# Optimization experiments

Hardware: AMD Instinct MI355X
Metric: run time of the kernel (lower is better)

Reference implementation:

```python
import jax, jax.numpy as jnp
import numpy as np

N_USERS = 100000
N_ITEMS = 50000
EMB_DIM = 64
N_LAYERS = 2
N_INTENTS = 128
N_EDGES = 4000000
N_NODES = N_USERS + N_ITEMS


def setup_inputs() -> dict:
    key = jax.random.key(0)
    k1, k2, k3, k4, k5 = jax.random.split(key, 5)
    return {
        "user_emb": 0.1 * jax.random.normal(k1, (N_USERS, EMB_DIM), dtype=jnp.float32),
        "item_emb": 0.1 * jax.random.normal(k2, (N_ITEMS, EMB_DIM), dtype=jnp.float32),
        "intents": jax.random.normal(k3, (EMB_DIM, N_INTENTS), dtype=jnp.float32) * (2.0 / (EMB_DIM + N_INTENTS)) ** 0.5,
        "h_idx": jax.random.randint(k4, (N_EDGES,), 0, N_NODES, dtype=jnp.int64)
        if jax.config.jax_enable_x64 else jax.random.randint(k4, (N_EDGES,), 0, N_NODES, dtype=jnp.int32),
        "t_idx": jax.random.randint(k5, (N_EDGES,), 0, N_NODES, dtype=jnp.int32),
    }


def _spmm(h_idx, t_idx, g_vals, x):
    # y[h] += g_vals * x[t]  (sparse matrix @ dense, COO form)
    gathered = x[t_idx] * g_vals[:, None]  # [E, D]
    return jax.ops.segment_sum(gathered, h_idx, num_segments=N_NODES)


def reference(user_emb, item_emb, intents, h_idx, t_idx):
    # --- _cal_sparse_adj: G = D^{-1/2} A D^{-1/2}, A values are ones ---
    deg = jax.ops.segment_sum(jnp.ones_like(h_idx, dtype=user_emb.dtype), h_idx,
                              num_segments=N_NODES)
    d_inv_sqrt = jnp.where(deg > 0, jax.lax.rsqrt(jnp.maximum(deg, 1e-12)), 0.0)
    g_vals = d_inv_sqrt[h_idx] * d_inv_sqrt[t_idx]  # [E]

    # --- multi-layer propagation with intent-aware embeddings ---
    embs = jnp.concatenate([user_emb, item_emb], axis=0)  # [N, D]
    all_embs = [embs]
    for _ in range(N_LAYERS):
        gnn_embs = _spmm(h_idx, t_idx, g_vals, embs)  # [N, D]
        # intent projection: softmax over intents, reconstruct in emb space
        u, it = embs[:N_USERS], embs[N_USERS:]
        u_int = jax.nn.softmax(u @ intents, axis=1) @ intents.T      # [n_users, D]
        i_int = jax.nn.softmax(it @ intents, axis=1) @ intents.T     # [n_items, D]
        int_embs = jnp.concatenate([u_int, i_int], axis=0)
        embs = gnn_embs + int_embs
        all_embs.append(embs)
    out = jnp.sum(jnp.stack(all_embs, axis=1), axis=1) / len(all_embs)  # mean over layers
    return out
```

## Files before the change

kernel.cpp:

```cpp
#include <hip/hip_runtime.h>
#include <math.h>

#define N_USERS 100000
#define N_ITEMS 50000
#define N_NODES 150000
#define EMB 64
#define NI 128
#define NUM_EDGES 4000000
#define NPAD 150016
#define NB 586
#define BSTRIDE 8192
#define ETILE 4096
#define EGRID ((NUM_EDGES + ETILE - 1) / ETILE)
#define NTILES (N_NODES / 16)
#define SBLK ((NTILES + 7) / 8)

typedef __attribute__((ext_vector_type(8))) short bf16x8;
typedef __attribute__((ext_vector_type(4))) float f32x4;

__device__ __forceinline__ unsigned short f2bf(float f) {
    unsigned int u = __float_as_uint(f);
    u += 0x7FFFu + ((u >> 16) & 1u);
    return (unsigned short)(u >> 16);
}
__device__ __forceinline__ float bflo(unsigned int u) { return __uint_as_float(u << 16); }
__device__ __forceinline__ float bfhi(unsigned int u) { return __uint_as_float(u & 0xFFFF0000u); }


__global__ __launch_bounds__(256) void bucket_scatter(const int* __restrict__ h,
                                                      const int* __restrict__ t,
                                                      int* __restrict__ gcur,
                                                      unsigned int* __restrict__ ebuf) {
    __shared__ int lc[NB];
    __shared__ int lbase[NB];
    __shared__ int lcur[NB];
    int tid = threadIdx.x;
    for (int i = tid; i < NB; i += 256) lc[i] = 0;
    __syncthreads();
    int base = blockIdx.x * ETILE;
#pragma unroll
    for (int k = 0; k < ETILE / 256; ++k) {
        int idx = base + k * 256 + tid;
        if (idx < NUM_EDGES) atomicAdd(&lc[h[idx] >> 8], 1);
    }
    __syncthreads();
    for (int i = tid; i < NB; i += 256) {
        int c = lc[i];
        lbase[i] = c ? (i * BSTRIDE + atomicAdd(&gcur[i], c)) : 0;
        lcur[i] = 0;
    }
    __syncthreads();
#pragma unroll
    for (int k = 0; k < ETILE / 256; ++k) {
        int idx = base + k * 256 + tid;
        if (idx < NUM_EDGES) {
            int hh = h[idx], tt = t[idx];
            int b = hh >> 8;
            int p = lbase[b] + atomicAdd(&lcur[b], 1);
            int lim = b * BSTRIDE + BSTRIDE - 1;
            p = (p <= lim) ? p : lim;
            ebuf[p] = ((unsigned int)(hh & 255) << 18) | (unsigned int)tt;
        }
    }
}


__global__ __launch_bounds__(256) void bucket_csr(const int* __restrict__ gcur,
                                                  unsigned int* __restrict__ ebuf,
                                                  int2* __restrict__ rmeta,
                                                  float* __restrict__ dinv) {
    __shared__ unsigned int in_s[BSTRIDE];
    __shared__ unsigned int out_s[BSTRIDE];
    __shared__ int cnt_s[256];
    __shared__ int base_s[256];
    __shared__ int sc[256];
    int b = blockIdx.x, tid = threadIdx.x;
    int s = b * BSTRIDE;
    int n = gcur[b];
    if (n > BSTRIDE) n = BSTRIDE;

    for (int i = tid; i < n; i += 256) in_s[i] = ebuf[s + i];
    cnt_s[tid] = 0;
    __syncthreads();
    for (int i = tid; i < n; i += 256) atomicAdd(&cnt_s[in_s[i] >> 18], 1);
    __syncthreads();

    int c = cnt_s[tid];
    sc[tid] = c;
    __syncthreads();
    for (int off = 1; off < 256; off <<= 1) {
        int tv = (tid >= off) ? sc[tid - off] : 0;
        __syncthreads();
        sc[tid] += tv;
        __syncthreads();
    }
    int excl = sc[tid] - c;
    base_s[tid] = excl;
    int node = (b << 8) + tid;
    rmeta[node] = make_int2(s + excl, c);
    dinv[node] = (c > 0) ? rsqrtf((float)c) : 0.0f;
    cnt_s[tid] = 0;
    __syncthreads();

    for (int i = tid; i < n; i += 256) {
        unsigned int q = in_s[i];
        int hl = (int)(q >> 18);
        int p = base_s[hl] + atomicAdd(&cnt_s[hl], 1);
        out_s[p] = q & 0x3FFFFu;
    }
    __syncthreads();
    for (int i = tid; i < n; i += 256) ebuf[s + i] = out_s[i];
}


__global__ void init_kernel(const float4* __restrict__ ue4, const float4* __restrict__ ie4,
                            uint2* __restrict__ ebf4, float4* __restrict__ out4) {
    int i = blockIdx.x * blockDim.x + threadIdx.x;
    const int uelems = N_USERS * EMB / 4;
    const int total  = N_NODES * EMB / 4;
    if (i < total) {
        float4 v = (i < uelems) ? ue4[i] : ie4[i - uelems];
        out4[i] = v;
        unsigned int p0 = ((unsigned int)f2bf(v.y) << 16) | f2bf(v.x);
        unsigned int p1 = ((unsigned int)f2bf(v.w) << 16) | f2bf(v.z);
        ebf4[i] = make_uint2(p0, p1);
    }
}


__global__ __launch_bounds__(512, 6) void spmm_intent(const int2* __restrict__ rmeta,
                                                      const unsigned int* __restrict__ col,
                                                      const float* __restrict__ dinv,
                                                      const unsigned short* __restrict__ ebf,
                                                      unsigned short* __restrict__ ebfout,
                                                      const float* __restrict__ W,
                                                      float* __restrict__ acc, float scale) {
    __shared__ __align__(16) unsigned short W1s[NI * 72];
    __shared__ __align__(16) unsigned short W2s[EMB * 136];
    __shared__ __align__(16) float UPool[8][520];

    int tid = threadIdx.x;

    const float4* W4 = (const float4*)W;
#pragma unroll
    for (int k = 0; k < 4; ++k) {
        int f = tid + k * 512;
        float4 v = W4[f];
        int d = f >> 5, c4 = (f & 31) << 2;
        unsigned short bx = f2bf(v.x), by = f2bf(v.y), bz = f2bf(v.z), bw = f2bf(v.w);
        *(unsigned int*)&W2s[d * 136 + c4]     = (unsigned int)bx | ((unsigned int)by << 16);
        *(unsigned int*)&W2s[d * 136 + c4 + 2] = (unsigned int)bz | ((unsigned int)bw << 16);
        W1s[(c4 + 0) * 72 + d] = bx;
        W1s[(c4 + 1) * 72 + d] = by;
        W1s[(c4 + 2) * 72 + d] = bz;
        W1s[(c4 + 3) * 72 + d] = bw;
    }
    __syncthreads();

    int wid = tid >> 6, lane = tid & 63;
    int q = lane >> 4, c = lane & 15;
    int qq = lane >> 3, cc = lane & 7;
    int tile = blockIdx.x * 8 + wid;
    if (tile >= NTILES) return;
    int rowbase = tile << 4;
    unsigned short* pw = (unsigned short*)&UPool[wid][0];
    float* fw = &UPool[wid][0];

    const unsigned short* erow = ebf + ((size_t)(rowbase + c) << 6);
    bf16x8 A0 = *(const bf16x8*)(erow + (q << 3));
    bf16x8 A1 = *(const bf16x8*)(erow + 32 + (q << 3));
    f32x4 S[8];
#pragma unroll
    for (int t = 0; t < 8; ++t) {
        bf16x8 B0 = *(const bf16x8*)&W1s[(16 * t + c) * 72 + (q << 3)];
        bf16x8 B1 = *(const bf16x8*)&W1s[(16 * t + c) * 72 + 32 + (q << 3)];
        f32x4 z = {0.f, 0.f, 0.f, 0.f};
        z = __builtin_amdgcn_mfma_f32_16x16x32_bf16(A0, B0, z, 0, 0, 0);
        S[t] = __builtin_amdgcn_mfma_f32_16x16x32_bf16(A1, B1, z, 0, 0, 0);
    }

#pragma unroll
    for (int r = 0; r < 4; ++r) {
        float m = S[0][r];
#pragma unroll
        for (int t = 1; t < 8; ++t) m = fmaxf(m, S[t][r]);
        m = fmaxf(m, __shfl_xor(m, 1)); m = fmaxf(m, __shfl_xor(m, 2));
        m = fmaxf(m, __shfl_xor(m, 4)); m = fmaxf(m, __shfl_xor(m, 8));
        float sum = 0.f;
#pragma unroll
        for (int t = 0; t < 8; ++t) { float ex = __expf(S[t][r] - m); S[t][r] = ex; sum += ex; }
        sum += __shfl_xor(sum, 1); sum += __shfl_xor(sum, 2);
        sum += __shfl_xor(sum, 4); sum += __shfl_xor(sum, 8);
        float inv = 1.0f / sum;
#pragma unroll
        for (int t = 0; t < 8; ++t) S[t][r] *= inv;
    }

    f32x4 O0 = {0.f, 0.f, 0.f, 0.f}, O1 = O0, O2 = O0, O3 = O0;
#pragma unroll
    for (int s2 = 0; s2 < 4; ++s2) {
#pragma unroll
        for (int h2 = 0; h2 < 2; ++h2) {
            int t = 2 * s2 + h2;
#pragma unroll
            for (int r = 0; r < 4; ++r) {
                float p = S[t][r];
                unsigned short b = f2bf(p);
                pw[(4 * q + r) * 40 + (h2 << 4) + c] = b;
                S[t][r] = p - bflo((unsigned int)b);
            }
        }
        bf16x8 Pf = *(const bf16x8*)&pw[c * 40 + (q << 3)];
        {
            bf16x8 Bf0 = *(const bf16x8*)&W2s[(c) * 136 + (s2 << 5) + (q << 3)];
            bf16x8 Bf1 = *(const bf16x8*)&W2s[(16 + c) * 136 + (s2 << 5) + (q << 3)];
            bf16x8 Bf2 = *(const bf16x8*)&W2s[(32 + c) * 136 + (s2 << 5) + (q << 3)];
            bf16x8 Bf3 = *(const bf16x8*)&W2s[(48 + c) * 136 + (s2 << 5) + (q << 3)];
            O0 = __builtin_amdgcn_mfma_f32_16x16x32_bf16(Pf, Bf0, O0, 0, 0, 0);
            O1 = __builtin_amdgcn_mfma_f32_16x16x32_bf16(Pf, Bf1, O1, 0, 0, 0);
            O2 = __builtin_amdgcn_mfma_f32_16x16x32_bf16(Pf, Bf2, O2, 0, 0, 0);
            O3 = __builtin_amdgcn_mfma_f32_16x16x32_bf16(Pf, Bf3, O3, 0, 0, 0);
        }
#pragma unroll
        for (int h2 = 0; h2 < 2; ++h2) {
            int t = 2 * s2 + h2;
#pragma unroll
            for (int r = 0; r < 4; ++r)
                pw[(4 * q + r) * 40 + (h2 << 4) + c] = f2bf(S[t][r]);
        }
        bf16x8 Pl = *(const bf16x8*)&pw[c * 40 + (q << 3)];
        {
            bf16x8 Bf0 = *(const bf16x8*)&W2s[(c) * 136 + (s2 << 5) + (q << 3)];
            bf16x8 Bf1 = *(const bf16x8*)&W2s[(16 + c) * 136 + (s2 << 5) + (q << 3)];
            bf16x8 Bf2 = *(const bf16x8*)&W2s[(32 + c) * 136 + (s2 << 5) + (q << 3)];
            bf16x8 Bf3 = *(const bf16x8*)&W2s[(48 + c) * 136 + (s2 << 5) + (q << 3)];
            O0 = __builtin_amdgcn_mfma_f32_16x16x32_bf16(Pl, Bf0, O0, 0, 0, 0);
            O1 = __builtin_amdgcn_mfma_f32_16x16x32_bf16(Pl, Bf1, O1, 0, 0, 0);
            O2 = __builtin_amdgcn_mfma_f32_16x16x32_bf16(Pl, Bf2, O2, 0, 0, 0);
            O3 = __builtin_amdgcn_mfma_f32_16x16x32_bf16(Pl, Bf3, O3, 0, 0, 0);
        }
    }

    asm volatile("" ::: "memory");

#pragma unroll 1
    for (int half = 0; half < 2; ++half) {
        int row = rowbase + half * 8 + qq;
        int2 rm = rmeta[row];
        int s = rm.x, deg = rm.y;
        float dr = dinv[row];
        int dm = deg;
        dm = max(dm, __shfl_xor(dm, 8));
        dm = max(dm, __shfl_xor(dm, 16));
        dm = max(dm, __shfl_xor(dm, 32));
        dm = __builtin_amdgcn_readfirstlane(dm);

        float a0 = 0.f, a1 = 0.f, a2 = 0.f, a3 = 0.f;
        float a4 = 0.f, a5 = 0.f, a6 = 0.f, a7 = 0.f;
        int last = s + ((deg > 0) ? (deg - 1) : 0);
        int i1 = s + 1; if (i1 > last) i1 = last;
        int ce0 = (int)col[s];
        int ce1 = (int)col[i1];
        float g0 = dinv[ce0], g1 = dinv[ce1];
        const unsigned short* eb = ebf + (cc << 3);
        for (int it = 0; it < dm; it += 2) {
            float gu0 = (it < deg) ? g0 : 0.f;
            float gu1 = (it + 1 < deg) ? g1 : 0.f;
            uint4 u0 = *(const uint4*)(eb + ((size_t)ce0 << 6));
            uint4 u1 = *(const uint4*)(eb + ((size_t)ce1 << 6));
            int p0 = s + it + 2; if (p0 > last) p0 = last;
            int p1 = s + it + 3; if (p1 > last) p1 = last;
            ce0 = (int)col[p0]; ce1 = (int)col[p1];
            g0 = dinv[ce0]; g1 = dinv[ce1];
            a0 = fmaf(gu0, bflo(u0.x), a0); a1 = fmaf(gu0, bfhi(u0.x), a1);
            a2 = fmaf(gu0, bflo(u0.y), a2); a3 = fmaf(gu0, bfhi(u0.y), a3);
            a4 = fmaf(gu0, bflo(u0.z), a4); a5 = fmaf(gu0, bfhi(u0.z), a5);
            a6 = fmaf(gu0, bflo(u0.w), a6); a7 = fmaf(gu0, bfhi(u0.w), a7);
            a0 = fmaf(gu1, bflo(u1.x), a0); a1 = fmaf(gu1, bfhi(u1.x), a1);
            a2 = fmaf(gu1, bflo(u1.y), a2); a3 = fmaf(gu1, bfhi(u1.y), a3);
            a4 = fmaf(gu1, bflo(u1.z), a4); a5 = fmaf(gu1, bfhi(u1.z), a5);
            a6 = fmaf(gu1, bflo(u1.w), a6); a7 = fmaf(gu1, bfhi(u1.w), a7);
        }
        int fb = qq * 65 + (cc << 3);
        fw[fb + 0] = a0 * dr; fw[fb + 1] = a1 * dr;
        fw[fb + 2] = a2 * dr; fw[fb + 3] = a3 * dr;
        fw[fb + 4] = a4 * dr; fw[fb + 5] = a5 * dr;
        fw[fb + 6] = a6 * dr; fw[fb + 7] = a7 * dr;

        if ((q >> 1) == half) {
            int qb = (q & 1) << 2;
#pragma unroll
            for (int r = 0; r < 4; ++r) {
                int rl = qb + r;
                const float* gr = &fw[rl * 65];
                size_t rbase = ((size_t)(rowbase + half * 8 + rl) << 6);
                float nv0 = gr[c]      + O0[r];
                float nv1 = gr[16 + c] + O1[r];
                float nv2 = gr[32 + c] + O2[r];
                float nv3 = gr[48 + c] + O3[r];
                ebfout[rbase + c]      = f2bf(nv0);
                ebfout[rbase + 16 + c] = f2bf(nv1);
                ebfout[rbase + 32 + c] = f2bf(nv2);
                ebfout[rbase + 48 + c] = f2bf(nv3);
                acc[rbase + c]      = (acc[rbase + c]      + nv0) * scale;
                acc[rbase + 16 + c] = (acc[rbase + 16 + c] + nv1) * scale;
                acc[rbase + 32 + c] = (acc[rbase + 32 + c] + nv2) * scale;
                acc[rbase + 48 + c] = (acc[rbase + 48 + c] + nv3) * scale;
            }
        }
    }
}


extern "C" void kernel_launch(void* const* d_in, const int* in_sizes, int n_in,
                              void* d_out, int out_size, void* d_ws, size_t ws_size,
                              hipStream_t stream) {
    const float* ue = (const float*)d_in[0];
    const float* ie = (const float*)d_in[1];
    const float* W  = (const float*)d_in[2];
    const int*   h  = (const int*)d_in[3];
    const int*   t  = (const int*)d_in[4];
    float* out = (float*)d_out;

    int*            gcur  = (int*)d_ws;
    int2*           rmeta = (int2*)(gcur + 1024);
    float*          dinv  = (float*)(rmeta + NPAD);
    unsigned int*   ebuf  = (unsigned int*)(dinv + NPAD);
    unsigned short* ebfA  = (unsigned short*)(ebuf + NB * BSTRIDE);
    unsigned short* ebfB  = ebfA + (size_t)NPAD * EMB;

    hipMemsetAsync(gcur, 0, NB * sizeof(int), stream);
    bucket_scatter<<<EGRID, 256, 0, stream>>>(h, t, gcur, ebuf);
    bucket_csr<<<NB, 256, 0, stream>>>(gcur, ebuf, rmeta, dinv);
    init_kernel<<<(N_NODES * EMB / 4 + 255) / 256, 256, 0, stream>>>(
        (const float4*)ue, (const float4*)ie, (uint2*)ebfA, (float4*)out);

    const unsigned int* col = ebuf;
    spmm_intent<<<SBLK, 512, 0, stream>>>(rmeta, col, dinv, ebfA, ebfB, W, out, 1.0f);
    spmm_intent<<<SBLK, 512, 0, stream>>>(rmeta, col, dinv, ebfB, ebfA, W, out, 1.0f / 3.0f);
}
```

Baseline: 435.9 us.

## Replace bucketed CSR build with atomic degree count and placement; move weights to global bf16

The two-pass bucketed CSR construction is replaced by a per-node degree-count kernel, a per-bucket scan kernel, and a direct atomic placement kernel. Intent weights are converted to bf16 once in a separate kernel and read from global memory instead of being staged into shared memory by every block. The spmm kernel now uses 256-thread blocks, unrolls the gather loop by four with clamped column indices, and runs the intent MFMA after the neighbour gather. Global atomics on per-node counters add contention and make edge order within a row nondeterministic. Dropping shared-memory weights cuts per-block setup but adds global/L2 traffic for weight fragments.

```diff
diff --git a/kernel.cpp b/kernel.cpp
--- a/kernel.cpp
+++ b/kernel.cpp
@@ -10,10 +10,9 @@
 #define NPAD 150016
 #define NB 586
 #define BSTRIDE 8192
-#define ETILE 4096
-#define EGRID ((NUM_EDGES + ETILE - 1) / ETILE)
 #define NTILES (N_NODES / 16)
-#define SBLK ((NTILES + 7) / 8)
+#define SBLK ((NTILES + 3) / 4)
+#define EDGE_BLOCKS ((NUM_EDGES + 255) / 256)
 
 typedef __attribute__((ext_vector_type(8))) short bf16x8;
 typedef __attribute__((ext_vector_type(4))) float f32x4;
@@ -27,65 +26,19 @@
 __device__ __forceinline__ float bfhi(unsigned int u) { return __uint_as_float(u & 0xFFFF0000u); }
 
 
-__global__ __launch_bounds__(256) void bucket_scatter(const int* __restrict__ h,
-                                                      const int* __restrict__ t,
-                                                      int* __restrict__ gcur,
-                                                      unsigned int* __restrict__ ebuf) {
-    __shared__ int lc[NB];
-    __shared__ int lbase[NB];
-    __shared__ int lcur[NB];
-    int tid = threadIdx.x;
-    for (int i = tid; i < NB; i += 256) lc[i] = 0;
-    __syncthreads();
-    int base = blockIdx.x * ETILE;
-#pragma unroll
-    for (int k = 0; k < ETILE / 256; ++k) {
-        int idx = base + k * 256 + tid;
-        if (idx < NUM_EDGES) atomicAdd(&lc[h[idx] >> 8], 1);
-    }
-    __syncthreads();
-    for (int i = tid; i < NB; i += 256) {
-        int c = lc[i];
-        lbase[i] = c ? (i * BSTRIDE + atomicAdd(&gcur[i], c)) : 0;
-        lcur[i] = 0;
-    }
-    __syncthreads();
-#pragma unroll
-    for (int k = 0; k < ETILE / 256; ++k) {
-        int idx = base + k * 256 + tid;
-        if (idx < NUM_EDGES) {
-            int hh = h[idx], tt = t[idx];
-            int b = hh >> 8;
-            int p = lbase[b] + atomicAdd(&lcur[b], 1);
-            int lim = b * BSTRIDE + BSTRIDE - 1;
-            p = (p <= lim) ? p : lim;
-            ebuf[p] = ((unsigned int)(hh & 255) << 18) | (unsigned int)tt;
-        }
-    }
-}
-
-
-__global__ __launch_bounds__(256) void bucket_csr(const int* __restrict__ gcur,
-                                                  unsigned int* __restrict__ ebuf,
-                                                  int2* __restrict__ rmeta,
-                                                  float* __restrict__ dinv) {
-    __shared__ unsigned int in_s[BSTRIDE];
-    __shared__ unsigned int out_s[BSTRIDE];
-    __shared__ int cnt_s[256];
-    __shared__ int base_s[256];
+__global__ __launch_bounds__(256) void deg_count(const int* __restrict__ h,
+                                                 int* __restrict__ deg) {
+    int i = blockIdx.x * 256 + threadIdx.x;
+    if (i < NUM_EDGES) atomicAdd(&deg[h[i]], 1);
+}
+
+__global__ __launch_bounds__(256) void node_meta(int* __restrict__ deg,
+                                                 int2* __restrict__ rmeta,
+                                                 float* __restrict__ dinv) {
     __shared__ int sc[256];
     int b = blockIdx.x, tid = threadIdx.x;
-    int s = b * BSTRIDE;
-    int n = gcur[b];
-    if (n > BSTRIDE) n = BSTRIDE;
-
-    for (int i = tid; i < n; i += 256) in_s[i] = ebuf[s + i];
-    cnt_s[tid] = 0;
-    __syncthreads();
-    for (int i = tid; i < n; i += 256) atomicAdd(&cnt_s[in_s[i] >> 18], 1);
-    __syncthreads();
-
-    int c = cnt_s[tid];
+    int node = (b << 8) + tid;
+    int c = (node < N_NODES) ? deg[node] : 0;
     sc[tid] = c;
     __syncthreads();
     for (int off = 1; off < 256; off <<= 1) {
@@ -94,22 +47,23 @@
         sc[tid] += tv;
         __syncthreads();
     }
-    int excl = sc[tid] - c;
-    base_s[tid] = excl;
-    int node = (b << 8) + tid;
-    rmeta[node] = make_int2(s + excl, c);
-    dinv[node] = (c > 0) ? rsqrtf((float)c) : 0.0f;
-    cnt_s[tid] = 0;
-    __syncthreads();
-
-    for (int i = tid; i < n; i += 256) {
-        unsigned int q = in_s[i];
-        int hl = (int)(q >> 18);
-        int p = base_s[hl] + atomicAdd(&cnt_s[hl], 1);
-        out_s[p] = q & 0x3FFFFu;
-    }
-    __syncthreads();
-    for (int i = tid; i < n; i += 256) ebuf[s + i] = out_s[i];
+    int start = b * BSTRIDE + (sc[tid] - c);
+    if (node < N_NODES) {
+        rmeta[node] = make_int2(start, c);
+        dinv[node] = (c > 0) ? rsqrtf((float)c) : 0.0f;
+        deg[node] = start;
+    }
+}
+
+__global__ __launch_bounds__(256) void place(const int* __restrict__ h,
+                                             const int* __restrict__ t,
+                                             int* __restrict__ cur,
+                                             unsigned int* __restrict__ ebuf) {
+    int i = blockIdx.x * 256 + threadIdx.x;
+    if (i < NUM_EDGES) {
+        int p = atomicAdd(&cur[h[i]], 1);
+        ebuf[p] = (unsigned int)t[i];
+    }
 }
 
 
@@ -128,120 +82,38 @@
 }
 
 
-__global__ __launch_bounds__(512, 6) void spmm_intent(const int2* __restrict__ rmeta,
+__global__ __launch_bounds__(256) void wconv(const float* __restrict__ W,
+                                             unsigned short* __restrict__ Wt,
+                                             unsigned short* __restrict__ W2b) {
+    int i = blockIdx.x * 256 + threadIdx.x;
+    if (i < EMB * NI) {
+        int d = i >> 7, c = i & 127;
+        unsigned short b = f2bf(W[i]);
+        W2b[i] = b;
+        Wt[c * EMB + d] = b;
+    }
+}
+
+
+__global__ __launch_bounds__(256, 7) void spmm_intent(const int2* __restrict__ rmeta,
                                                       const unsigned int* __restrict__ col,
                                                       const float* __restrict__ dinv,
                                                       const unsigned short* __restrict__ ebf,
                                                       unsigned short* __restrict__ ebfout,
-                                                      const float* __restrict__ W,
+                                                      const unsigned short* __restrict__ Wt,
+                                                      const unsigned short* __restrict__ W2b,
                                                       float* __restrict__ acc, float scale) {
-    __shared__ __align__(16) unsigned short W1s[NI * 72];
-    __shared__ __align__(16) unsigned short W2s[EMB * 136];
-    __shared__ __align__(16) float UPool[8][520];
+    __shared__ __align__(16) float UPool[4][1408];
 
     int tid = threadIdx.x;
-
-    const float4* W4 = (const float4*)W;
-#pragma unroll
-    for (int k = 0; k < 4; ++k) {
-        int f = tid + k * 512;
-        float4 v = W4[f];
-        int d = f >> 5, c4 = (f & 31) << 2;
-        unsigned short bx = f2bf(v.x), by = f2bf(v.y), bz = f2bf(v.z), bw = f2bf(v.w);
-        *(unsigned int*)&W2s[d * 136 + c4]     = (unsigned int)bx | ((unsigned int)by << 16);
-        *(unsigned int*)&W2s[d * 136 + c4 + 2] = (unsigned int)bz | ((unsigned int)bw << 16);
-        W1s[(c4 + 0) * 72 + d] = bx;
-        W1s[(c4 + 1) * 72 + d] = by;
-        W1s[(c4 + 2) * 72 + d] = bz;
-        W1s[(c4 + 3) * 72 + d] = bw;
-    }
-    __syncthreads();
-
     int wid = tid >> 6, lane = tid & 63;
     int q = lane >> 4, c = lane & 15;
     int qq = lane >> 3, cc = lane & 7;
-    int tile = blockIdx.x * 8 + wid;
+    int tile = blockIdx.x * 4 + wid;
     if (tile >= NTILES) return;
     int rowbase = tile << 4;
-    unsigned short* pw = (unsigned short*)&UPool[wid][0];
     float* fw = &UPool[wid][0];
-
-    const unsigned short* erow = ebf + ((size_t)(rowbase + c) << 6);
-    bf16x8 A0 = *(const bf16x8*)(erow + (q << 3));
-    bf16x8 A1 = *(const bf16x8*)(erow + 32 + (q << 3));
-    f32x4 S[8];
-#pragma unroll
-    for (int t = 0; t < 8; ++t) {
-        bf16x8 B0 = *(const bf16x8*)&W1s[(16 * t + c) * 72 + (q << 3)];
-        bf16x8 B1 = *(const bf16x8*)&W1s[(16 * t + c) * 72 + 32 + (q << 3)];
-        f32x4 z = {0.f, 0.f, 0.f, 0.f};
-        z = __builtin_amdgcn_mfma_f32_16x16x32_bf16(A0, B0, z, 0, 0, 0);
-        S[t] = __builtin_amdgcn_mfma_f32_16x16x32_bf16(A1, B1, z, 0, 0, 0);
-    }
-
-#pragma unroll
-    for (int r = 0; r < 4; ++r) {
-        float m = S[0][r];
-#pragma unroll
-        for (int t = 1; t < 8; ++t) m = fmaxf(m, S[t][r]);
-        m = fmaxf(m, __shfl_xor(m, 1)); m = fmaxf(m, __shfl_xor(m, 2));
-        m = fmaxf(m, __shfl_xor(m, 4)); m = fmaxf(m, __shfl_xor(m, 8));
-        float sum = 0.f;
-#pragma unroll
-        for (int t = 0; t < 8; ++t) { float ex = __expf(S[t][r] - m); S[t][r] = ex; sum += ex; }
-        sum += __shfl_xor(sum, 1); sum += __shfl_xor(sum, 2);
-        sum += __shfl_xor(sum, 4); sum += __shfl_xor(sum, 8);
-        float inv = 1.0f / sum;
-#pragma unroll
-        for (int t = 0; t < 8; ++t) S[t][r] *= inv;
-    }
-
-    f32x4 O0 = {0.f, 0.f, 0.f, 0.f}, O1 = O0, O2 = O0, O3 = O0;
-#pragma unroll
-    for (int s2 = 0; s2 < 4; ++s2) {
-#pragma unroll
-        for (int h2 = 0; h2 < 2; ++h2) {
-            int t = 2 * s2 + h2;
-#pragma unroll
-            for (int r = 0; r < 4; ++r) {
-                float p = S[t][r];
-                unsigned short b = f2bf(p);
-                pw[(4 * q + r) * 40 + (h2 << 4) + c] = b;
-                S[t][r] = p - bflo((unsigned int)b);
-            }
-        }
-        bf16x8 Pf = *(const bf16x8*)&pw[c * 40 + (q << 3)];
-        {
-            bf16x8 Bf0 = *(const bf16x8*)&W2s[(c) * 136 + (s2 << 5) + (q << 3)];
-            bf16x8 Bf1 = *(const bf16x8*)&W2s[(16 + c) * 136 + (s2 << 5) + (q << 3)];
-            bf16x8 Bf2 = *(const bf16x8*)&W2s[(32 + c) * 136 + (s2 << 5) + (q << 3)];
-            bf16x8 Bf3 = *(const bf16x8*)&W2s[(48 + c) * 136 + (s2 << 5) + (q << 3)];
-            O0 = __builtin_amdgcn_mfma_f32_16x16x32_bf16(Pf, Bf0, O0, 0, 0, 0);
-            O1 = __builtin_amdgcn_mfma_f32_16x16x32_bf16(Pf, Bf1, O1, 0, 0, 0);
-            O2 = __builtin_amdgcn_mfma_f32_16x16x32_bf16(Pf, Bf2, O2, 0, 0, 0);
-            O3 = __builtin_amdgcn_mfma_f32_16x16x32_bf16(Pf, Bf3, O3, 0, 0, 0);
-        }
-#pragma unroll
-        for (int h2 = 0; h2 < 2; ++h2) {
-            int t = 2 * s2 + h2;
-#pragma unroll
-            for (int r = 0; r < 4; ++r)
-                pw[(4 * q + r) * 40 + (h2 << 4) + c] = f2bf(S[t][r]);
-        }
-        bf16x8 Pl = *(const bf16x8*)&pw[c * 40 + (q << 3)];
-        {
-            bf16x8 Bf0 = *(const bf16x8*)&W2s[(c) * 136 + (s2 << 5) + (q << 3)];
-            bf16x8 Bf1 = *(const bf16x8*)&W2s[(16 + c) * 136 + (s2 << 5) + (q << 3)];
-            bf16x8 Bf2 = *(const bf16x8*)&W2s[(32 + c) * 136 + (s2 << 5) + (q << 3)];
-            bf16x8 Bf3 = *(const bf16x8*)&W2s[(48 + c) * 136 + (s2 << 5) + (q << 3)];
-            O0 = __builtin_amdgcn_mfma_f32_16x16x32_bf16(Pl, Bf0, O0, 0, 0, 0);
-            O1 = __builtin_amdgcn_mfma_f32_16x16x32_bf16(Pl, Bf1, O1, 0, 0, 0);
-            O2 = __builtin_amdgcn_mfma_f32_16x16x32_bf16(Pl, Bf2, O2, 0, 0, 0);
-            O3 = __builtin_amdgcn_mfma_f32_16x16x32_bf16(Pl, Bf3, O3, 0, 0, 0);
-        }
-    }
-
-    asm volatile("" ::: "memory");
+    unsigned short* pw = (unsigned short*)&UPool[wid][1088];
 
 #pragma unroll 1
     for (int half = 0; half < 2; ++half) {
@@ -258,20 +130,28 @@
         float a0 = 0.f, a1 = 0.f, a2 = 0.f, a3 = 0.f;
         float a4 = 0.f, a5 = 0.f, a6 = 0.f, a7 = 0.f;
         int last = s + ((deg > 0) ? (deg - 1) : 0);
-        int i1 = s + 1; if (i1 > last) i1 = last;
-        int ce0 = (int)col[s];
-        int ce1 = (int)col[i1];
-        float g0 = dinv[ce0], g1 = dinv[ce1];
+        int ce0 = min((int)col[s], N_NODES - 1);
+        int ce1 = min((int)col[min(s + 1, last)], N_NODES - 1);
+        int ce2 = min((int)col[min(s + 2, last)], N_NODES - 1);
+        int ce3 = min((int)col[min(s + 3, last)], N_NODES - 1);
+        float g0 = dinv[ce0], g1 = dinv[ce1], g2 = dinv[ce2], g3 = dinv[ce3];
         const unsigned short* eb = ebf + (cc << 3);
-        for (int it = 0; it < dm; it += 2) {
+        for (int it = 0; it < dm; it += 4) {
             float gu0 = (it < deg) ? g0 : 0.f;
             float gu1 = (it + 1 < deg) ? g1 : 0.f;
+            float gu2 = (it + 2 < deg) ? g2 : 0.f;
+            float gu3 = (it + 3 < deg) ? g3 : 0.f;
             uint4 u0 = *(const uint4*)(eb + ((size_t)ce0 << 6));
             uint4 u1 = *(const uint4*)(eb + ((size_t)ce1 << 6));
-            int p0 = s + it + 2; if (p0 > last) p0 = last;
-            int p1 = s + it + 3; if (p1 > last) p1 = last;
-            ce0 = (int)col[p0]; ce1 = (int)col[p1];
-            g0 = dinv[ce0]; g1 = dinv[ce1];
+            uint4 u2 = *(const uint4*)(eb + ((size_t)ce2 << 6));
+            uint4 u3 = *(const uint4*)(eb + ((size_t)ce3 << 6));
+            int p0 = min(s + it + 4, last), p1 = min(s + it + 5, last);
+            int p2 = min(s + it + 6, last), p3 = min(s + it + 7, last);
+            ce0 = min((int)col[p0], N_NODES - 1);
+            ce1 = min((int)col[p1], N_NODES - 1);
+            ce2 = min((int)col[p2], N_NODES - 1);
+            ce3 = min((int)col[p3], N_NODES - 1);
+            g0 = dinv[ce0]; g1 = dinv[ce1]; g2 = dinv[ce2]; g3 = dinv[ce3];
             a0 = fmaf(gu0, bflo(u0.x), a0); a1 = fmaf(gu0, bfhi(u0.x), a1);
             a2 = fmaf(gu0, bflo(u0.y), a2); a3 = fmaf(gu0, bfhi(u0.y), a3);
             a4 = fmaf(gu0, bflo(u0.z), a4); a5 = fmaf(gu0, bfhi(u0.z), a5);
@@ -280,34 +160,116 @@
             a2 = fmaf(gu1, bflo(u1.y), a2); a3 = fmaf(gu1, bfhi(u1.y), a3);
             a4 = fmaf(gu1, bflo(u1.z), a4); a5 = fmaf(gu1, bfhi(u1.z), a5);
             a6 = fmaf(gu1, bflo(u1.w), a6); a7 = fmaf(gu1, bfhi(u1.w), a7);
-        }
-        int fb = qq * 65 + (cc << 3);
+            a0 = fmaf(gu2, bflo(u2.x), a0); a1 = fmaf(gu2, bfhi(u2.x), a1);
+            a2 = fmaf(gu2, bflo(u2.y), a2); a3 = fmaf(gu2, bfhi(u2.y), a3);
+            a4 = fmaf(gu2, bflo(u2.z), a4); a5 = fmaf(gu2, bfhi(u2.z), a5);
+            a6 = fmaf(gu2, bflo(u2.w), a6); a7 = fmaf(gu2, bfhi(u2.w), a7);
+            a0 = fmaf(gu3, bflo(u3.x), a0); a1 = fmaf(gu3, bfhi(u3.x), a1);
+            a2 = fmaf(gu3, bflo(u3.y), a2); a3 = fmaf(gu3, bfhi(u3.y), a3);
+            a4 = fmaf(gu3, bflo(u3.z), a4); a5 = fmaf(gu3, bfhi(u3.z), a5);
+            a6 = fmaf(gu3, bflo(u3.w), a6); a7 = fmaf(gu3, bfhi(u3.w), a7);
+        }
+        int fb = (half * 8 + qq) * 68 + (cc << 3);
         fw[fb + 0] = a0 * dr; fw[fb + 1] = a1 * dr;
         fw[fb + 2] = a2 * dr; fw[fb + 3] = a3 * dr;
         fw[fb + 4] = a4 * dr; fw[fb + 5] = a5 * dr;
         fw[fb + 6] = a6 * dr; fw[fb + 7] = a7 * dr;
-
-        if ((q >> 1) == half) {
-            int qb = (q & 1) << 2;
+    }
+
+    const unsigned short* erow = ebf + ((size_t)(rowbase + c) << 6);
+    bf16x8 A0 = *(const bf16x8*)(erow + (q << 3));
+    bf16x8 A1 = *(const bf16x8*)(erow + 32 + (q << 3));
+    f32x4 S[8];
+#pragma unroll
+    for (int t = 0; t < 8; ++t) {
+        bf16x8 B0 = *(const bf16x8*)&Wt[(16 * t + c) * EMB + (q << 3)];
+        bf16x8 B1 = *(const bf16x8*)&Wt[(16 * t + c) * EMB + 32 + (q << 3)];
+        f32x4 z = {0.f, 0.f, 0.f, 0.f};
+        z = __builtin_amdgcn_mfma_f32_16x16x32_bf16(A0, B0, z, 0, 0, 0);
+        S[t] = __builtin_amdgcn_mfma_f32_16x16x32_bf16(A1, B1, z, 0, 0, 0);
+    }
+
+#pragma unroll
+    for (int r = 0; r < 4; ++r) {
+        float m = S[0][r];
+#pragma unroll
+        for (int t = 1; t < 8; ++t) m = fmaxf(m, S[t][r]);
+        m = fmaxf(m, __shfl_xor(m, 1)); m = fmaxf(m, __shfl_xor(m, 2));
+        m = fmaxf(m, __shfl_xor(m, 4)); m = fmaxf(m, __shfl_xor(m, 8));
+        float sum = 0.f;
+#pragma unroll
+        for (int t = 0; t < 8; ++t) { float ex = __expf(S[t][r] - m); S[t][r] = ex; sum += ex; }
+        sum += __shfl_xor(sum, 1); sum += __shfl_xor(sum, 2);
+        sum += __shfl_xor(sum, 4); sum += __shfl_xor(sum, 8);
+        float inv = 1.0f / sum;
+#pragma unroll
+        for (int t = 0; t < 8; ++t) S[t][r] *= inv;
+    }
+
+    f32x4 O0 = {0.f, 0.f, 0.f, 0.f}, O1 = O0, O2 = O0, O3 = O0;
+#pragma unroll
+    for (int s2 = 0; s2 < 4; ++s2) {
+#pragma unroll
+        for (int h2 = 0; h2 < 2; ++h2) {
+            int t = 2 * s2 + h2;
 #pragma unroll
             for (int r = 0; r < 4; ++r) {
-                int rl = qb + r;
-                const float* gr = &fw[rl * 65];
-                size_t rbase = ((size_t)(rowbase + half * 8 + rl) << 6);
-                float nv0 = gr[c]      + O0[r];
-                float nv1 = gr[16 + c] + O1[r];
-                float nv2 = gr[32 + c] + O2[r];
-                float nv3 = gr[48 + c] + O3[r];
-                ebfout[rbase + c]      = f2bf(nv0);
-                ebfout[rbase + 16 + c] = f2bf(nv1);
-                ebfout[rbase + 32 + c] = f2bf(nv2);
-                ebfout[rbase + 48 + c] = f2bf(nv3);
-                acc[rbase + c]      = (acc[rbase + c]      + nv0) * scale;
-                acc[rbase + 16 + c] = (acc[rbase + 16 + c] + nv1) * scale;
-                acc[rbase + 32 + c] = (acc[rbase + 32 + c] + nv2) * scale;
-                acc[rbase + 48 + c] = (acc[rbase + 48 + c] + nv3) * scale;
+                float p = S[t][r];
+                unsigned short b = f2bf(p);
+                pw[(4 * q + r) * 40 + (h2 << 4) + c] = b;
+                S[t][r] = p - bflo((unsigned int)b);
             }
         }
+        bf16x8 Pf = *(const bf16x8*)&pw[c * 40 + (q << 3)];
+        {
+            bf16x8 Bf0 = *(const bf16x8*)&W2b[(c) * NI + (s2 << 5) + (q << 3)];
+            bf16x8 Bf1 = *(const bf16x8*)&W2b[(16 + c) * NI + (s2 << 5) + (q << 3)];
+            O0 = __builtin_amdgcn_mfma_f32_16x16x32_bf16(Pf, Bf0, O0, 0, 0, 0);
+            O1 = __builtin_amdgcn_mfma_f32_16x16x32_bf16(Pf, Bf1, O1, 0, 0, 0);
+            bf16x8 Bf2 = *(const bf16x8*)&W2b[(32 + c) * NI + (s2 << 5) + (q << 3)];
+            bf16x8 Bf3 = *(const bf16x8*)&W2b[(48 + c) * NI + (s2 << 5) + (q << 3)];
+            O2 = __builtin_amdgcn_mfma_f32_16x16x32_bf16(Pf, Bf2, O2, 0, 0, 0);
+            O3 = __builtin_amdgcn_mfma_f32_16x16x32_bf16(Pf, Bf3, O3, 0, 0, 0);
+        }
+#pragma unroll
+        for (int h2 = 0; h2 < 2; ++h2) {
+            int t = 2 * s2 + h2;
+#pragma unroll
+            for (int r = 0; r < 4; ++r)
+                pw[(4 * q + r) * 40 + (h2 << 4) + c] = f2bf(S[t][r]);
+        }
+        bf16x8 Pl = *(const bf16x8*)&pw[c * 40 + (q << 3)];
+        {
+            bf16x8 Bf0 = *(const bf16x8*)&W2b[(c) * NI + (s2 << 5) + (q << 3)];
+            bf16x8 Bf1 = *(const bf16x8*)&W2b[(16 + c) * NI + (s2 << 5) + (q << 3)];
+            O0 = __builtin_amdgcn_mfma_f32_16x16x32_bf16(Pl, Bf0, O0, 0, 0, 0);
+            O1 = __builtin_amdgcn_mfma_f32_16x16x32_bf16(Pl, Bf1, O1, 0, 0, 0);
+            bf16x8 Bf2 = *(const bf16x8*)&W2b[(32 + c) * NI + (s2 << 5) + (q << 3)];
+            bf16x8 Bf3 = *(const bf16x8*)&W2b[(48 + c) * NI + (s2 << 5) + (q << 3)];
+            O2 = __builtin_amdgcn_mfma_f32_16x16x32_bf16(Pl, Bf2, O2, 0, 0, 0);
+            O3 = __builtin_amdgcn_mfma_f32_16x16x32_bf16(Pl, Bf3, O3, 0, 0, 0);
+        }
+    }
+
+    asm volatile("" ::: "memory");
+
+#pragma unroll
+    for (int r = 0; r < 4; ++r) {
+        int rl = 4 * q + r;
+        const float* gr = &fw[rl * 68];
+        size_t rbase = ((size_t)(rowbase + rl) << 6);
+        float nv0 = gr[c]      + O0[r];
+        float nv1 = gr[16 + c] + O1[r];
+        float nv2 = gr[32 + c] + O2[r];
+        float nv3 = gr[48 + c] + O3[r];
+        ebfout[rbase + c]      = f2bf(nv0);
+        ebfout[rbase + 16 + c] = f2bf(nv1);
+        ebfout[rbase + 32 + c] = f2bf(nv2);
+        ebfout[rbase + 48 + c] = f2bf(nv3);
+        acc[rbase + c]      = (acc[rbase + c]      + nv0) * scale;
+        acc[rbase + 16 + c] = (acc[rbase + 16 + c] + nv1) * scale;
+        acc[rbase + 32 + c] = (acc[rbase + 32 + c] + nv2) * scale;
+        acc[rbase + 48 + c] = (acc[rbase + 48 + c] + nv3) * scale;
     }
 }
 
@@ -322,20 +284,24 @@
     const int*   t  = (const int*)d_in[4];
     float* out = (float*)d_out;
 
-    int*            gcur  = (int*)d_ws;
-    int2*           rmeta = (int2*)(gcur + 1024);
+    int*            deg   = (int*)d_ws;
+    int2*           rmeta = (int2*)(deg + NPAD);
     float*          dinv  = (float*)(rmeta + NPAD);
     unsigned int*   ebuf  = (unsigned int*)(dinv + NPAD);
-    unsigned short* ebfA  = (unsigned short*)(ebuf + NB * BSTRIDE);
+    unsigned short* Wt    = (unsigned short*)(ebuf + NB * BSTRIDE);
+    unsigned short* W2b   = Wt + EMB * NI;
+    unsigned short* ebfA  = W2b + EMB * NI;
     unsigned short* ebfB  = ebfA + (size_t)NPAD * EMB;
 
-    hipMemsetAsync(gcur, 0, NB * sizeof(int), stream);
-    bucket_scatter<<<EGRID, 256, 0, stream>>>(h, t, gcur, ebuf);
-    bucket_csr<<<NB, 256, 0, stream>>>(gcur, ebuf, rmeta, dinv);
+    hipMemsetAsync(deg, 0, N_NODES * sizeof(int), stream);
+    deg_count<<<EDGE_BLOCKS, 256, 0, stream>>>(h, deg);
+    node_meta<<<NB, 256, 0, stream>>>(deg, rmeta, dinv);
+    place<<<EDGE_BLOCKS, 256, 0, stream>>>(h, t, deg, ebuf);
     init_kernel<<<(N_NODES * EMB / 4 + 255) / 256, 256, 0, stream>>>(
         (const float4*)ue, (const float4*)ie, (uint2*)ebfA, (float4*)out);
+    wconv<<<(EMB * NI + 255) / 256, 256, 0, stream>>>(W, Wt, W2b);
 
     const unsigned int* col = ebuf;
-    spmm_intent<<<SBLK, 512, 0, stream>>>(rmeta, col, dinv, ebfA, ebfB, W, out, 1.0f);
-    spmm_intent<<<SBLK, 512, 0, stream>>>(rmeta, col, dinv, ebfB, ebfA, W, out, 1.0f / 3.0f);
-}
+    spmm_intent<<<SBLK, 256, 0, stream>>>(rmeta, col, dinv, ebfA, ebfB, Wt, W2b, out, 1.0f);
+    spmm_intent<<<SBLK, 256, 0, stream>>>(rmeta, col, dinv, ebfB, ebfA, Wt, W2b, out, 1.0f / 3.0f);
+}
```

Measured after the change: 860.2 us. 1.97x slower.
